# Performance work log

Measured on AMD Instinct MI355X. Metric: run time of the kernel, lower is better.

## Reference

```python
import jax, jax.numpy as jnp
import numpy as np

F = 32          # field_size == len(feature_sizes) == mpl_dims[0]
V = 10000       # per-field vocab
D = 496         # embedding_size == comb(F, 2)
H = 1024        # mpl_dims[1]
OUT = 1         # mpl_dims[-1]
B = 16384


def setup_inputs() -> dict:
    key = jax.random.key(0)
    ks = jax.random.split(key, 8)
    xv = jax.random.normal(ks[0], (B, F), dtype=jnp.float32)
    xi = jax.random.randint(ks[1], (B, F), 0, V, dtype=jnp.int64)
    # stacked per-field embedding tables: [F, V, D]
    emb = jax.random.normal(ks[2], (F, V, D), dtype=jnp.float32) * 0.05
    W1 = jax.random.normal(ks[3], (F, H), dtype=jnp.float32) * (1.0 / np.sqrt(F))
    b1 = jax.random.normal(ks[4], (H,), dtype=jnp.float32) * 0.01
    W2 = jax.random.normal(ks[5], (H + D, OUT), dtype=jnp.float32) * (1.0 / np.sqrt(H + D))
    b2 = jax.random.normal(ks[6], (OUT,), dtype=jnp.float32) * 0.01
    return {"xv": xv, "xi": xi, "emb": emb, "W1": W1, "b1": b1, "W2": W2, "b2": b2}


def reference(xv, xi, emb, W1, b1, W2, b2):
    # Per-field embedding gather, scaled by the field value: e[b,f,:] = emb[f, xi[b,f], :] * xv[b,f]
    gathered = jax.vmap(lambda table, idx: table[idx], in_axes=(0, 1), out_axes=1)(emb, xi)  # [B, F, D]
    e = gathered * xv[:, :, None]
    # FM sum-square minus square-sum interaction -> [B, D]
    s = jnp.sum(e, axis=1)
    qi = 0.5 * (s * s - jnp.sum(e * e, axis=1))
    # MLP branch on raw values (dropout inactive at inference)
    h = jax.nn.relu(xv @ W1 + b1)  # [B, H]
    x = jnp.concatenate([qi, h], axis=1)  # [B, D + H]
    return x @ W2 + b2  # [B, OUT]
```

## Files before the change

kernel.cpp:

```cpp
#include <hip/hip_runtime.h>

constexpr int F  = 32;
constexpr int V  = 10000;
constexpr int D  = 496;
constexpr int H  = 1024;
constexpr int NT = 128;

__global__ __launch_bounds__(NT, 4) void deepqi_fused(
    const float* __restrict__ xv,
    const int*   __restrict__ xi,
    const float* __restrict__ emb,
    const float* __restrict__ W1,
    const float* __restrict__ b1,
    const float* __restrict__ W2,
    const float* __restrict__ b2,
    float* __restrict__ out)
{
    const int b = blockIdx.x;
    const int t = threadIdx.x;

    __shared__ float        s_xv[F];
    __shared__ const float* s_row[F];
    __shared__ float        s_wsum[NT / 64];

    if (t < F) {
        s_xv[t]  = xv[b * F + t];
        s_row[t] = emb + ((size_t)t * V + (size_t)xi[b * F + t]) * D;
    }
    __syncthreads();

    float acc = 0.0f;

    if (t < D / 4) {
        float4 s  = make_float4(0.f, 0.f, 0.f, 0.f);
        float4 ss = make_float4(0.f, 0.f, 0.f, 0.f);
        #pragma unroll 8
        for (int f = 0; f < F; ++f) {
            const float xf = s_xv[f];
            float4 v = *reinterpret_cast<const float4*>(s_row[f] + 4 * t);
            v.x *= xf; v.y *= xf; v.z *= xf; v.w *= xf;
            s.x  += v.x;       s.y  += v.y;       s.z  += v.z;       s.w  += v.w;
            ss.x += v.x * v.x; ss.y += v.y * v.y; ss.z += v.z * v.z; ss.w += v.w * v.w;
        }
        float4 w = *reinterpret_cast<const float4*>(W2 + 4 * t);
        float qx = 0.5f * (s.x * s.x - ss.x);
        float qy = 0.5f * (s.y * s.y - ss.y);
        float qz = 0.5f * (s.z * s.z - ss.z);
        float qw = 0.5f * (s.w * s.w - ss.w);
        acc = qx * w.x + qy * w.y + qz * w.z + qw * w.w;
    }

    {
        const int j0 = 8 * t;
        float4 ba = *reinterpret_cast<const float4*>(b1 + j0);
        float4 bb = *reinterpret_cast<const float4*>(b1 + j0 + 4);
        float h0 = ba.x, h1 = ba.y, h2 = ba.z, h3 = ba.w;
        float h4 = bb.x, h5 = bb.y, h6 = bb.z, h7 = bb.w;
        #pragma unroll 4
        for (int f = 0; f < F; ++f) {
            const float xf = s_xv[f];
            float4 wa = *reinterpret_cast<const float4*>(W1 + f * H + j0);
            float4 wb = *reinterpret_cast<const float4*>(W1 + f * H + j0 + 4);
            h0 += xf * wa.x; h1 += xf * wa.y; h2 += xf * wa.z; h3 += xf * wa.w;
            h4 += xf * wb.x; h5 += xf * wb.y; h6 += xf * wb.z; h7 += xf * wb.w;
        }
        float4 wa = *reinterpret_cast<const float4*>(W2 + D + j0);
        float4 wb = *reinterpret_cast<const float4*>(W2 + D + j0 + 4);
        acc += fmaxf(h0, 0.f) * wa.x + fmaxf(h1, 0.f) * wa.y
             + fmaxf(h2, 0.f) * wa.z + fmaxf(h3, 0.f) * wa.w
             + fmaxf(h4, 0.f) * wb.x + fmaxf(h5, 0.f) * wb.y
             + fmaxf(h6, 0.f) * wb.z + fmaxf(h7, 0.f) * wb.w;
    }

    #pragma unroll
    for (int off = 32; off > 0; off >>= 1)
        acc += __shfl_down(acc, off, 64);
    if ((t & 63) == 0) s_wsum[t >> 6] = acc;
    __syncthreads();
    if (t == 0) out[b] = s_wsum[0] + s_wsum[1] + b2[0];
}

extern "C" void kernel_launch(void* const* d_in, const int* in_sizes, int n_in,
                              void* d_out, int out_size, void* d_ws, size_t ws_size,
                              hipStream_t stream) {
    const float* xv  = (const float*)d_in[0];
    const int*   xi  = (const int*)d_in[1];
    const float* emb = (const float*)d_in[2];
    const float* W1  = (const float*)d_in[3];
    const float* b1  = (const float*)d_in[4];
    const float* W2  = (const float*)d_in[5];
    const float* b2  = (const float*)d_in[6];
    float* out = (float*)d_out;

    const int B = in_sizes[0] / F;
    deepqi_fused<<<B, NT, 0, stream>>>(xv, xi, emb, W1, b1, W2, b2, out);
}
```

Before: 891.1 us.

## Split FM gather and MLP into separate kernels with batched W1 reuse

Splits the fused per-row kernel into two kernels. The first does the FM embedding gather and interaction, with higher occupancy bounds. The second computes the MLP branch over tiles of 64 rows, so each W1 value is reused across 8 rows held in registers instead of being reloaded for every batch row. The MLP kernel adds its partial result into the output with a read-modify-write. This relies on the two kernels running in order on the same stream, and it adds a second launch plus extra global writes.

```diff
diff --git a/kernel.cpp b/kernel.cpp
--- a/kernel.cpp
+++ b/kernel.cpp
@@ -4,14 +4,11 @@
 constexpr int V  = 10000;
 constexpr int D  = 496;
 constexpr int H  = 1024;
-constexpr int NT = 128;
 
-__global__ __launch_bounds__(NT, 4) void deepqi_fused(
+__global__ __launch_bounds__(128, 8) void fm_kernel(
     const float* __restrict__ xv,
     const int*   __restrict__ xi,
     const float* __restrict__ emb,
-    const float* __restrict__ W1,
-    const float* __restrict__ b1,
     const float* __restrict__ W2,
     const float* __restrict__ b2,
     float* __restrict__ out)
@@ -21,7 +18,7 @@
 
     __shared__ float        s_xv[F];
     __shared__ const float* s_row[F];
-    __shared__ float        s_wsum[NT / 64];
+    __shared__ float        s_wsum[2];
 
     if (t < F) {
         s_xv[t]  = xv[b * F + t];
@@ -30,11 +27,10 @@
     __syncthreads();
 
     float acc = 0.0f;
-
     if (t < D / 4) {
         float4 s  = make_float4(0.f, 0.f, 0.f, 0.f);
         float4 ss = make_float4(0.f, 0.f, 0.f, 0.f);
-        #pragma unroll 8
+        #pragma unroll 4
         for (int f = 0; f < F; ++f) {
             const float xf = s_xv[f];
             float4 v = *reinterpret_cast<const float4*>(s_row[f] + 4 * t);
@@ -43,33 +39,10 @@
             ss.x += v.x * v.x; ss.y += v.y * v.y; ss.z += v.z * v.z; ss.w += v.w * v.w;
         }
         float4 w = *reinterpret_cast<const float4*>(W2 + 4 * t);
-        float qx = 0.5f * (s.x * s.x - ss.x);
-        float qy = 0.5f * (s.y * s.y - ss.y);
-        float qz = 0.5f * (s.z * s.z - ss.z);
-        float qw = 0.5f * (s.w * s.w - ss.w);
-        acc = qx * w.x + qy * w.y + qz * w.z + qw * w.w;
-    }
-
-    {
-        const int j0 = 8 * t;
-        float4 ba = *reinterpret_cast<const float4*>(b1 + j0);
-        float4 bb = *reinterpret_cast<const float4*>(b1 + j0 + 4);
-        float h0 = ba.x, h1 = ba.y, h2 = ba.z, h3 = ba.w;
-        float h4 = bb.x, h5 = bb.y, h6 = bb.z, h7 = bb.w;
-        #pragma unroll 4
-        for (int f = 0; f < F; ++f) {
-            const float xf = s_xv[f];
-            float4 wa = *reinterpret_cast<const float4*>(W1 + f * H + j0);
-            float4 wb = *reinterpret_cast<const float4*>(W1 + f * H + j0 + 4);
-            h0 += xf * wa.x; h1 += xf * wa.y; h2 += xf * wa.z; h3 += xf * wa.w;
-            h4 += xf * wb.x; h5 += xf * wb.y; h6 += xf * wb.z; h7 += xf * wb.w;
-        }
-        float4 wa = *reinterpret_cast<const float4*>(W2 + D + j0);
-        float4 wb = *reinterpret_cast<const float4*>(W2 + D + j0 + 4);
-        acc += fmaxf(h0, 0.f) * wa.x + fmaxf(h1, 0.f) * wa.y
-             + fmaxf(h2, 0.f) * wa.z + fmaxf(h3, 0.f) * wa.w
-             + fmaxf(h4, 0.f) * wb.x + fmaxf(h5, 0.f) * wb.y
-             + fmaxf(h6, 0.f) * wb.z + fmaxf(h7, 0.f) * wb.w;
+        acc = (0.5f * (s.x * s.x - ss.x)) * w.x
+            + (0.5f * (s.y * s.y - ss.y)) * w.y
+            + (0.5f * (s.z * s.z - ss.z)) * w.z
+            + (0.5f * (s.w * s.w - ss.w)) * w.w;
     }
 
     #pragma unroll
@@ -78,6 +51,77 @@
     if ((t & 63) == 0) s_wsum[t >> 6] = acc;
     __syncthreads();
     if (t == 0) out[b] = s_wsum[0] + s_wsum[1] + b2[0];
+}
+
+constexpr int R  = 64;
+constexpr int RC = 8;
+
+__global__ __launch_bounds__(256, 4) void mlp_kernel(
+    const float* __restrict__ xv,
+    const float* __restrict__ W1,
+    const float* __restrict__ b1,
+    const float* __restrict__ W2,
+    float* __restrict__ out,
+    int B)
+{
+    const int t  = threadIdx.x;
+    const int b0 = blockIdx.x * R;
+    const int j0 = 4 * t;
+
+    __shared__ float s_xv[F][R];
+    __shared__ float s_red[RC][4];
+
+    {
+        const int r0 = t >> 3, f0 = 4 * (t & 7);
+        const int rA = min(b0 + r0,      B - 1);
+        const int rB = min(b0 + r0 + 32, B - 1);
+        float4 v0 = *reinterpret_cast<const float4*>(xv + (size_t)rA * F + f0);
+        float4 v1 = *reinterpret_cast<const float4*>(xv + (size_t)rB * F + f0);
+        s_xv[f0 + 0][r0] = v0.x; s_xv[f0 + 1][r0] = v0.y;
+        s_xv[f0 + 2][r0] = v0.z; s_xv[f0 + 3][r0] = v0.w;
+        s_xv[f0 + 0][r0 + 32] = v1.x; s_xv[f0 + 1][r0 + 32] = v1.y;
+        s_xv[f0 + 2][r0 + 32] = v1.z; s_xv[f0 + 3][r0 + 32] = v1.w;
+    }
+    __syncthreads();
+
+    const float4 w2v = *reinterpret_cast<const float4*>(W2 + D + j0);
+    const float4 bv  = *reinterpret_cast<const float4*>(b1 + j0);
+
+    for (int rc = 0; rc < R; rc += RC) {
+        float4 h[RC];
+        #pragma unroll
+        for (int r = 0; r < RC; ++r) h[r] = bv;
+
+        #pragma unroll 4
+        for (int f = 0; f < F; ++f) {
+            const float4 w  = *reinterpret_cast<const float4*>(W1 + f * H + j0);
+            const float4 xa = *reinterpret_cast<const float4*>(&s_xv[f][rc]);
+            const float4 xb = *reinterpret_cast<const float4*>(&s_xv[f][rc + 4]);
+            const float xr[RC] = {xa.x, xa.y, xa.z, xa.w, xb.x, xb.y, xb.z, xb.w};
+            #pragma unroll
+            for (int r = 0; r < RC; ++r) {
+                h[r].x += xr[r] * w.x; h[r].y += xr[r] * w.y;
+                h[r].z += xr[r] * w.z; h[r].w += xr[r] * w.w;
+            }
+        }
+
+        #pragma unroll
+        for (int r = 0; r < RC; ++r) {
+            float p = fmaxf(h[r].x, 0.f) * w2v.x + fmaxf(h[r].y, 0.f) * w2v.y
+                    + fmaxf(h[r].z, 0.f) * w2v.z + fmaxf(h[r].w, 0.f) * w2v.w;
+            #pragma unroll
+            for (int off = 32; off > 0; off >>= 1)
+                p += __shfl_down(p, off, 64);
+            if ((t & 63) == 0) s_red[r][t >> 6] = p;
+        }
+        __syncthreads();
+        if (t < RC) {
+            const int row = b0 + rc + t;
+            if (row < B)
+                out[row] += s_red[t][0] + s_red[t][1] + s_red[t][2] + s_red[t][3];
+        }
+        __syncthreads();
+    }
 }
 
 extern "C" void kernel_launch(void* const* d_in, const int* in_sizes, int n_in,
@@ -93,5 +137,7 @@
     float* out = (float*)d_out;
 
     const int B = in_sizes[0] / F;
-    deepqi_fused<<<B, NT, 0, stream>>>(xv, xi, emb, W1, b1, W2, b2, out);
+
+    fm_kernel<<<B, 128, 0, stream>>>(xv, xi, emb, W2, b2, out);
+    mlp_kernel<<<(B + R - 1) / R, 256, 0, stream>>>(xv, W1, b1, W2, out, B);
 }
```

After: 880.2 us. About the same (-1.2%).
